# Performance work log

Hardware: AMD Instinct MI355X
Metric: run time of the kernel (lower is better)

## Reference

```python
import math
import jax, jax.numpy as jnp
import numpy as np

N = 100_000          # nodes
D = 128              # sample.num_node_features
E = 1_600_000        # edges (avg degree 16)
ACM = 4              # augmented_channels_multiplier
C = 128              # channels = 4*4*channels_optuna(=8)
RATIO = 0.7          # topk_ratio + 0.1
FINAL_NODES = 3


def setup_inputs() -> dict:
    key = jax.random.key(0)
    ks = jax.random.split(key, 14)
    s = 0.05
    x = jax.random.normal(ks[0], (N, D), jnp.float32)
    edge_index = jax.random.randint(ks[1], (2, E), 0, N, dtype=jnp.int32)
    # dense_input GraphConv(D, ACM): called with empty edges -> only lin_root weight + lin_rel bias matter
    Wd_root = jax.random.normal(ks[2], (ACM, D), jnp.float32) * s
    bd = jax.random.normal(ks[3], (ACM,), jnp.float32) * s
    # input GraphConv(ACM, C)
    Wi_rel = jax.random.normal(ks[4], (C, ACM), jnp.float32) * s
    bi = jax.random.normal(ks[5], (C,), jnp.float32) * s
    Wi_root = jax.random.normal(ks[6], (C, ACM), jnp.float32) * s
    # TopKPooling(C) attention vector
    p = jax.random.normal(ks[7], (C,), jnp.float32) * s
    # conv1 GraphConv(C, 2C)
    W1_rel = jax.random.normal(ks[8], (2 * C, C), jnp.float32) * s
    b1 = jax.random.normal(ks[9], (2 * C,), jnp.float32) * s
    W1_root = jax.random.normal(ks[10], (2 * C, C), jnp.float32) * s
    # output Linear(3 * 2C, 1)
    Wo = jax.random.normal(ks[11], (1, FINAL_NODES * 2 * C), jnp.float32) * s
    bo = jax.random.normal(ks[12], (1,), jnp.float32) * s
    return {"x": x, "edge_index": edge_index, "Wd_root": Wd_root, "bd": bd,
            "Wi_rel": Wi_rel, "bi": bi, "Wi_root": Wi_root, "p": p,
            "W1_rel": W1_rel, "b1": b1, "W1_root": W1_root, "Wo": Wo, "bo": bo}


def reference(x, edge_index, Wd_root, bd, Wi_rel, bi, Wi_root, p, W1_rel, b1, W1_root, Wo, bo):
    n = x.shape[0]
    src, dst = edge_index[0], edge_index[1]  # messages flow src -> dst

    # dense_input GraphConv with empty edge set: aggr == 0 -> lin_rel bias + lin_root(x)
    h = jax.nn.gelu(x @ Wd_root.T + bd, approximate=False)               # [N, ACM]

    # input GraphConv(ACM, C): out = lin_rel(sum_j x_j) + lin_root(x)
    aggr = jax.ops.segment_sum(h[src], dst, num_segments=n)              # [N, ACM]
    h = jax.nn.gelu(aggr @ Wi_rel.T + bi + h @ Wi_root.T, approximate=False)  # [N, C]

    # TopKPooling(C, ratio=0.7): score = tanh(x.p / ||p||), keep top-k, scale kept x by score
    k = int(math.ceil(RATIO * n))
    score = jnp.tanh((h @ p) / jnp.linalg.norm(p))                        # [N]
    top_scores, perm = jax.lax.top_k(score, k)
    hp = h[perm] * top_scores[:, None]                                    # [k, C]
    # remap edges: kept node -> new index, dropped -> sentinel k
    inv = jnp.full((n,), k, dtype=jnp.int32).at[perm].set(jnp.arange(k, dtype=jnp.int32))
    ns, nd = inv[src], inv[dst]
    valid = (ns < k) & (nd < k)

    # conv1 GraphConv(C, 2C) on coarsened graph (masked scatter, sentinel row dropped)
    msg = jnp.where(valid[:, None], hp[jnp.minimum(ns, k - 1)], 0.0)      # [E, C]
    aggr = jax.ops.segment_sum(msg, jnp.where(valid, nd, k), num_segments=k + 1)[:k]
    h2 = jax.nn.gelu(aggr @ W1_rel.T + b1 + hp @ W1_root.T, approximate=False)  # [k, 2C]

    # avg_pool_x with cluster = i % 3 over single-graph batch
    cluster = jnp.arange(k, dtype=jnp.int32) % FINAL_NODES
    sums = jax.ops.segment_sum(h2, cluster, num_segments=FINAL_NODES)
    counts = jax.ops.segment_sum(jnp.ones((k,), h2.dtype), cluster, num_segments=FINAL_NODES)
    pooled = sums / counts[:, None]                                       # [3, 2C]

    # output Linear on flattened vector -> shape [1]
    return pooled.reshape(-1) @ Wo.T + bo
```

## Files before the change

### kernel.cpp

```cpp
#include <hip/hip_runtime.h>
#include <stdint.h>

#define N_NODES 100000
#define D_FEAT  128
#define E_EDGES 1600000
#define ACMC    4
#define CCH     128
#define C2CH    256
#define KKEEP   70000
#define KPAD    70016
#define NBLK    547
#define BINCAP  64
#define NBINS   (1 << 20)
#define NWIN    8
#define WWIN    12500

#define NB_BUILD (1563 * NWIN)
#define NB_H1    (N_NODES / 4)
#define NB_WCONV 128
#define NB_FRONT (NB_BUILD + NB_H1 + NB_WCONV)

#define NB_GATHER ((N_NODES + 3) / 4)
#define NB_PACK   ((KPAD + 3) / 4)
#define NB_GP     (NB_GATHER + NB_PACK)

typedef unsigned int u32;
typedef unsigned long long u64;
typedef unsigned short u16;
typedef short bf16x8 __attribute__((ext_vector_type(8)));
typedef float f32x4 __attribute__((ext_vector_type(4)));
typedef int i32x4 __attribute__((ext_vector_type(4)));

__device__ __forceinline__ float gelu_exact(float v){
    return 0.5f * v * (1.0f + erff(v * 0.70710678118654752440f));
}
__device__ __forceinline__ float bflo(u32 v){ return __uint_as_float(v << 16); }
__device__ __forceinline__ float bfhi(u32 v){ return __uint_as_float(v & 0xFFFF0000u); }
__device__ __forceinline__ u16 f2bf(float f){
    u32 x = __float_as_uint(f);
    return (u16)((x + 0x7FFFu + ((x >> 16) & 1u)) >> 16);
}

__global__ __launch_bounds__(256) void k_front(const int* __restrict__ ei,
                                               int* __restrict__ deg,
                                               int* __restrict__ slot,
                                               const float* __restrict__ x,
                                               const float* __restrict__ Wd,
                                               const float* __restrict__ bd,
                                               float* __restrict__ h1,
                                               const float* __restrict__ Wrel,
                                               const float* __restrict__ Wroot,
                                               u16* __restrict__ wcat) {
    int b = blockIdx.x;
    if (b < NB_BUILD) {
        int win = b & (NWIN - 1);
        int chunk = b >> 3;
        int e0 = (chunk * 256 + threadIdx.x) * 4;
        if (e0 >= E_EDGES) return;
        i32x4 dv = __builtin_nontemporal_load((const i32x4*)(ei + E_EDGES + e0));
        i32x4 sv = __builtin_nontemporal_load((const i32x4*)(ei + e0));
        int lo = win * WWIN, hi = lo + WWIN;
        #pragma unroll
        for (int j = 0; j < 4; j++) {
            int d = dv[j];
            if (d >= lo && d < hi) {
                int pos = atomicAdd(&deg[d], 1);
                if (pos < BINCAP) slot[d * BINCAP + pos] = sv[j];
            }
        }
        return;
    }
    if (b < NB_BUILD + NB_H1) {
        int tid = threadIdx.x;
        int wid = tid >> 6, lane = tid & 63;
        int node = (b - NB_BUILD) * 4 + wid;
        const float2* xr = (const float2*)(x + (size_t)node * D_FEAT);
        float2 v = xr[lane];
        const float2* wd = (const float2*)Wd;
        float s[4];
        #pragma unroll
        for (int j = 0; j < 4; j++) {
            float2 w = wd[j * 64 + lane];
            s[j] = v.x * w.x + v.y * w.y;
        }
        #pragma unroll
        for (int off = 32; off > 0; off >>= 1) {
            #pragma unroll
            for (int j = 0; j < 4; j++) s[j] += __shfl_xor(s[j], off);
        }
        if (lane == 0) {
            float4 o;
            o.x = gelu_exact(s[0] + bd[0]);
            o.y = gelu_exact(s[1] + bd[1]);
            o.z = gelu_exact(s[2] + bd[2]);
            o.w = gelu_exact(s[3] + bd[3]);
            ((float4*)h1)[node] = o;
        }
        return;
    }
    {
        int g = (b - NB_BUILD - NB_H1) * 256 + threadIdx.x;
        int ch = g >> 7, t = g & 127;
        wcat[(size_t)ch * 256 + t]       = f2bf(Wrel[(size_t)ch * 128 + t]);
        wcat[(size_t)ch * 256 + 128 + t] = f2bf(Wroot[(size_t)ch * 128 + t]);
    }
}

__global__ __launch_bounds__(256) void k_aggr1g(const int* __restrict__ deg,
                                                const int* __restrict__ slot,
                                                const float* __restrict__ h1,
                                                float* __restrict__ aggr1) {
    int d = blockIdx.x * blockDim.x + threadIdx.x;
    if (d >= N_NODES) return;
    int cnt = deg[d]; if (cnt > BINCAP) cnt = BINCAP;
    int base = d * BINCAP;
    float4 acc = make_float4(0.f, 0.f, 0.f, 0.f);
    for (int i0 = 0; i0 < cnt; i0 += 8) {
        int m = cnt - i0; if (m > 8) m = 8;
        int ss[8];
        #pragma unroll
        for (int j = 0; j < 8; j++) {
            int sj = slot[base + i0 + j];
            ss[j] = (j < m) ? sj : 0;
        }
        float4 vv[8];
        #pragma unroll
        for (int j = 0; j < 8; j++) vv[j] = ((const float4*)h1)[ss[j]];
        #pragma unroll
        for (int j = 0; j < 8; j++) {
            float msk = (j < m) ? 1.f : 0.f;
            acc.x += msk * vv[j].x;
            acc.y += msk * vv[j].y;
            acc.z += msk * vv[j].z;
            acc.w += msk * vv[j].w;
        }
    }
    ((float4*)aggr1)[d] = acc;
}

__global__ __launch_bounds__(256) void k_h_score(const float* __restrict__ aggr1,
                                                 const float* __restrict__ h1,
                                                 const float* __restrict__ Wi_rel,
                                                 const float* __restrict__ bi,
                                                 const float* __restrict__ Wi_root,
                                                 const float* __restrict__ p,
                                                 u16* __restrict__ hsb,
                                                 u32* __restrict__ dkey,
                                                 int* __restrict__ hist) {
    __shared__ float4 swr[128], swo[128];
    __shared__ float sbi[128], spv[128];
    __shared__ float spred[2];
    __shared__ float red[2][2];
    __shared__ float sscore[2];
    int tid = threadIdx.x;
    if (tid < 128) {
        swr[tid] = ((const float4*)Wi_rel)[tid];
        swo[tid] = ((const float4*)Wi_root)[tid];
        sbi[tid] = bi[tid];
        spv[tid] = p[tid];
    }
    __syncthreads();
    if (tid < 128) {
        float pp = spv[tid] * spv[tid];
        #pragma unroll
        for (int off = 32; off > 0; off >>= 1) pp += __shfl_xor(pp, off);
        if ((tid & 63) == 0) spred[tid >> 6] = pp;
    }
    __syncthreads();
    float pnorm = sqrtf(spred[0] + spred[1]);

    int half = tid >> 7;
    int c = tid & 127;
    int wih = (tid >> 6) & 1;
    int lane = tid & 63;
    float4 wr = swr[c], wo = swo[c];
    float bic = sbi[c], pc = spv[c];

    for (int node = blockIdx.x * 2 + half; node < N_NODES; node += gridDim.x * 2) {
        float4 ag = ((const float4*)aggr1)[node];
        float4 hv = ((const float4*)h1)[node];
        float val = ag.x * wr.x + ag.y * wr.y + ag.z * wr.z + ag.w * wr.w
                  + hv.x * wo.x + hv.y * wo.y + hv.z * wo.z + hv.w * wo.w
                  + bic;
        float g = gelu_exact(val);
        float hp = g * pc;
        #pragma unroll
        for (int off = 32; off > 0; off >>= 1) hp += __shfl_xor(hp, off);
        if (lane == 0) red[half][wih] = hp;
        __syncthreads();
        if (c == 0) {
            float H = red[half][0] + red[half][1];
            float sc = tanhf(H / pnorm);
            sscore[half] = sc;
            u32 u = __float_as_uint(sc);
            u32 asc = (u & 0x80000000u) ? ~u : (u | 0x80000000u);
            u32 d = ~asc;
            dkey[node] = d;
            atomicAdd(&hist[d >> 12], 1);
        }
        __syncthreads();
        hsb[(size_t)node * CCH + c] = f2bf(g * sscore[half]);
        __syncthreads();
    }
}

__global__ __launch_bounds__(256) void k_escan1(const int* __restrict__ in,
                                                int* __restrict__ out,
                                                int* __restrict__ bsum,
                                                int n) {
    __shared__ int wsum[4];
    int tid = threadIdx.x;
    int lane = tid & 63, wave = tid >> 6;
    int base = blockIdx.x * 4096 + tid * 16;
    int o[16];
    #pragma unroll
    for (int i = 0; i < 16; i++) {
        int g = base + i;
        o[i] = (g < n) ? in[g] : 0;
    }
    int ex[16];
    int run = 0;
    #pragma unroll
    for (int i = 0; i < 16; i++) { ex[i] = run; run += o[i]; }
    int inc = run;
    #pragma unroll
    for (int off = 1; off < 64; off <<= 1) {
        int t = __shfl_up(inc, off);
        if (lane >= off) inc += t;
    }
    int wexc = inc - run;
    if (lane == 63) wsum[wave] = inc;
    __syncthreads();
    int wbase = 0;
    #pragma unroll
    for (int w = 0; w < 4; w++) wbase += (w < wave) ? wsum[w] : 0;
    int tbase = wbase + wexc;
    #pragma unroll
    for (int i = 0; i < 16; i++) {
        int g = base + i;
        if (g < n) out[g] = tbase + ex[i];
    }
    if (tid == 255) bsum[blockIdx.x] = wbase + inc;
}

__global__ __launch_bounds__(256) void k_escan2(int* __restrict__ bsum, int n) {
    __shared__ int wsum[4];
    int tid = threadIdx.x;
    int lane = tid & 63, wave = tid >> 6;
    int val = (tid < n) ? bsum[tid] : 0;
    int inc = val;
    #pragma unroll
    for (int off = 1; off < 64; off <<= 1) {
        int t = __shfl_up(inc, off);
        if (lane >= off) inc += t;
    }
    int wexc = inc - val;
    if (lane == 63) wsum[wave] = inc;
    __syncthreads();
    int wbase = 0;
    #pragma unroll
    for (int w = 0; w < 4; w++) wbase += (w < wave) ? wsum[w] : 0;
    if (tid < n) bsum[tid] = wbase + wexc;
}

__global__ __launch_bounds__(256) void k_escan3(int* __restrict__ out,
                                                const int* __restrict__ bsum,
                                                int n) {
    int add = bsum[blockIdx.x];
    int base = blockIdx.x * 4096 + threadIdx.x * 16;
    #pragma unroll
    for (int i = 0; i < 16; i++) {
        int g = base + i;
        if (g < n) out[g] += add;
    }
}

__global__ __launch_bounds__(256) void k_scatter(const u32* __restrict__ dkey,
                                                 int* __restrict__ cursor,
                                                 u64* __restrict__ out64) {
    int i = blockIdx.x * blockDim.x + threadIdx.x;
    if (i >= N_NODES) return;
    u32 d = dkey[i];
    int pos = atomicAdd(&cursor[d >> 12], 1);
    out64[pos] = (((u64)d) << 32) | (u32)i;
}

__global__ __launch_bounds__(256) void k_refine(const u64* __restrict__ out64,
                                                const int* __restrict__ cursor,
                                                const int* __restrict__ hist,
                                                int* __restrict__ rank,
                                                int* __restrict__ noder) {
    int pp = blockIdx.x * blockDim.x + threadIdx.x;
    if (pp >= N_NODES) return;
    u64 kp = out64[pp];
    u32 b = (u32)(kp >> 44);
    int end = cursor[b];
    int cnt = hist[b];
    int start = end - cnt;
    int r = start;
    if (cnt > 1) {
        int c = 0;
        for (int q = start; q < end; q++) c += (out64[q] < kp) ? 1 : 0;
        r = start + c;
    }
    int node = (int)(u32)kp;
    rank[node] = r;
    noder[r] = node;
}

__global__ __launch_bounds__(256) void k_gatherpack(const int* __restrict__ deg,
                                                    const int* __restrict__ slot,
                                                    const int* __restrict__ rank,
                                                    const int* __restrict__ noder,
                                                    const u32* __restrict__ hsb32,
                                                    u32* __restrict__ inb32) {
    int b = blockIdx.x;
    int tid = threadIdx.x;
    int wid = tid >> 6, lane = tid & 63;
    if (b < NB_GATHER) {
        int d = b * 4 + wid;
        if (d >= N_NODES) return;
        int rd = rank[d];
        if (rd >= KKEEP) return;
        int cnt = deg[d]; if (cnt > BINCAP) cnt = BINCAP;
        int base = d * BINCAP;
        float ax = 0.f, ay = 0.f;
        for (int i0 = 0; i0 < cnt; i0 += 16) {
            int m = cnt - i0; if (m > 16) m = 16;
            int ss[16];
            #pragma unroll
            for (int j = 0; j < 16; j++) {
                int sj = slot[base + i0 + j];
                ss[j] = (j < m) ? sj : 0;
            }
            int rr[16];
            u32 vv[16];
            #pragma unroll
            for (int j = 0; j < 16; j++) {
                rr[j] = rank[ss[j]];
                vv[j] = hsb32[(size_t)ss[j] * 64 + lane];
            }
            #pragma unroll
            for (int j = 0; j < 16; j++) {
                float msk = (j < m && rr[j] < KKEEP) ? 1.f : 0.f;
                ax += msk * bflo(vv[j]);
                ay += msk * bfhi(vv[j]);
            }
        }
        inb32[(size_t)rd * 128 + lane] = (u32)f2bf(ax) | ((u32)f2bf(ay) << 16);
        return;
    }
    {
        int r = (b - NB_GATHER) * 4 + wid;
        if (r >= KPAD) return;
        if (r < KKEEP) {
            int n = noder[r];
            inb32[(size_t)r * 128 + 64 + lane] = hsb32[(size_t)n * 64 + lane];
        } else {
            inb32[(size_t)r * 128 + lane] = 0;
            inb32[(size_t)r * 128 + 64 + lane] = 0;
        }
    }
}

__global__ __launch_bounds__(256, 2) void k_h2mfma(const u16* __restrict__ inb,
                                                   const u16* __restrict__ wcat,
                                                   const float* __restrict__ b1,
                                                   float* __restrict__ partial) {
    __shared__ u16 bs[128 * 256];
    __shared__ float ps[384];
    int tid = threadIdx.x;
    int rowt = blockIdx.x >> 1;
    int half = blockIdx.x & 1;
    int chbase = half * 128;

    {
        int lch = tid >> 1;
        int seg = tid & 1;
        const char* src = (const char*)wcat + (size_t)(chbase + lch) * 512 + seg * 256;
        char* dst = (char*)bs + (size_t)lch * 512;
        int swz = (lch & 7) << 4;
        #pragma unroll
        for (int i = 0; i < 16; i++) {
            int k = seg * 256 + i * 16;
            *(i32x4*)(dst + (k ^ swz)) = *(const i32x4*)(src + i * 16);
        }
    }
    for (int i = tid; i < 384; i += 256) ps[i] = 0.f;
    __syncthreads();

    int lane = tid & 63, wave = tid >> 6;
    int col = lane & 15, quad = lane >> 4;
    int rbase = rowt * 128 + wave * 32;

    bf16x8 a[2][8];
    #pragma unroll
    for (int m = 0; m < 2; m++) {
        const char* ar = (const char*)inb + (size_t)(rbase + m * 16 + col) * 512 + quad * 16;
        #pragma unroll
        for (int k0 = 0; k0 < 8; k0++)
            a[m][k0] = *(const bf16x8*)(ar + k0 * 64);
    }

    f32x4 acc[2][8];
    #pragma unroll
    for (int m = 0; m < 2; m++)
        #pragma unroll
        for (int n = 0; n < 8; n++)
            acc[m][n] = (f32x4){0.f, 0.f, 0.f, 0.f};

    int swzr = (col & 7) << 4;
    #pragma unroll
    for (int k0 = 0; k0 < 8; k0++) {
        int kb = k0 * 64 + quad * 16;
        bf16x8 b[8];
        #pragma unroll
        for (int n = 0; n < 8; n++) {
            int lch = n * 16 + col;
            b[n] = *(const bf16x8*)((const char*)bs + (size_t)lch * 512 + (kb ^ swzr));
        }
        #pragma unroll
        for (int n = 0; n < 8; n++) {
            acc[0][n] = __builtin_amdgcn_mfma_f32_16x16x32_bf16(a[0][k0], b[n], acc[0][n], 0, 0, 0);
            acc[1][n] = __builtin_amdgcn_mfma_f32_16x16x32_bf16(a[1][k0], b[n], acc[1][n], 0, 0, 0);
        }
    }

    #pragma unroll
    for (int m = 0; m < 2; m++) {
        #pragma unroll
        for (int n = 0; n < 8; n++) {
            int lch = n * 16 + col;
            float bias = b1[chbase + lch];
            float p0 = 0.f, p1 = 0.f, p2 = 0.f;
            #pragma unroll
            for (int reg = 0; reg < 4; reg++) {
                int r = rbase + m * 16 + quad * 4 + reg;
                float g = (r < KKEEP) ? gelu_exact(acc[m][n][reg] + bias) : 0.f;
                int md = r % 3;
                if (md == 0) p0 += g; else if (md == 1) p1 += g; else p2 += g;
            }
            p0 += __shfl_xor(p0, 16); p0 += __shfl_xor(p0, 32);
            p1 += __shfl_xor(p1, 16); p1 += __shfl_xor(p1, 32);
            p2 += __shfl_xor(p2, 16); p2 += __shfl_xor(p2, 32);
            if (quad == 0) {
                atomicAdd(&ps[0 * 128 + lch], p0);
                atomicAdd(&ps[1 * 128 + lch], p1);
                atomicAdd(&ps[2 * 128 + lch], p2);
            }
        }
    }
    __syncthreads();
    for (int i = tid; i < 384; i += 256)
        partial[(size_t)rowt * 768 + (i >> 7) * 256 + chbase + (i & 127)] = ps[i];
}

__global__ __launch_bounds__(256) void k_poolred(const float* __restrict__ partial,
                                                 float* __restrict__ pooled) {
    __shared__ float red[4][64];
    int tid = threadIdx.x, lane = tid & 63, wave = tid >> 6;
    int j = blockIdx.x * 64 + lane;
    float s = 0.f;
    for (int i = wave; i < NBLK; i += 4)
        s += partial[(size_t)i * 768 + j];
    red[wave][lane] = s;
    __syncthreads();
    if (wave == 0)
        pooled[j] = (red[0][lane] + red[1][lane]) + (red[2][lane] + red[3][lane]);
}

__global__ __launch_bounds__(768) void k_out(const float* __restrict__ pooled,
                                             const float* __restrict__ Wo,
                                             const float* __restrict__ bo,
                                             float* __restrict__ out) {
    __shared__ float red[12];
    int t = threadIdx.x;
    int ci = t >> 8;
    float cnt = (ci == 0) ? 23334.0f : 23333.0f;
    float acc = (pooled[t] / cnt) * Wo[t];
    #pragma unroll
    for (int off = 32; off > 0; off >>= 1) acc += __shfl_xor(acc, off);
    int wid = t >> 6, lane = t & 63;
    if (lane == 0) red[wid] = acc;
    __syncthreads();
    if (t == 0) {
        float s = 0.0f;
        #pragma unroll
        for (int w = 0; w < 12; w++) s += red[w];
        out[0] = s + bo[0];
    }
}

extern "C" void kernel_launch(void* const* d_in, const int* in_sizes, int n_in,
                              void* d_out, int out_size, void* d_ws, size_t ws_size,
                              hipStream_t stream) {
    const float* x       = (const float*)d_in[0];
    const int*   ei      = (const int*)d_in[1];
    const float* Wd      = (const float*)d_in[2];
    const float* bd      = (const float*)d_in[3];
    const float* Wi_rel  = (const float*)d_in[4];
    const float* bi      = (const float*)d_in[5];
    const float* Wi_root = (const float*)d_in[6];
    const float* p       = (const float*)d_in[7];
    const float* W1_rel  = (const float*)d_in[8];
    const float* b1      = (const float*)d_in[9];
    const float* W1_root = (const float*)d_in[10];
    const float* Wo      = (const float*)d_in[11];
    const float* bo      = (const float*)d_in[12];

    char* ws = (char*)d_ws;
    size_t off_b = 0;
    auto alloc = [&](size_t bytes) -> void* {
        void* ptr = ws + off_b;
        off_b += (bytes + 255) & ~(size_t)255;
        return ptr;
    };
    float* h1     = (float*)alloc((size_t)N_NODES * 4 * sizeof(float));
    float* aggr1  = (float*)alloc((size_t)N_NODES * 4 * sizeof(float));
    u16*   hsb    = (u16*)alloc((size_t)N_NODES * CCH * sizeof(u16));
    u32*   dkey   = (u32*)alloc((size_t)N_NODES * sizeof(u32));
    int*   rank   = (int*)alloc((size_t)N_NODES * sizeof(int));
    int*   noder  = (int*)alloc((size_t)N_NODES * sizeof(int));
    int*   deg    = (int*)alloc((size_t)N_NODES * sizeof(int));
    int*   slot   = (int*)alloc((size_t)N_NODES * BINCAP * sizeof(int));
    u16*   inb    = (u16*)alloc((size_t)KPAD * C2CH * sizeof(u16));
    u16*   wcat   = (u16*)alloc((size_t)C2CH * 256 * sizeof(u16));
    float* partial= (float*)alloc((size_t)NBLK * 768 * sizeof(float));
    float* pooled = (float*)alloc(768 * sizeof(float));
    (void)ws_size; (void)in_sizes; (void)n_in; (void)out_size;

    int* hist   = (int*)inb;
    int* cursor = (int*)inb + NBINS;
    u64* out64  = (u64*)((int*)inb + 2 * NBINS);
    int* bsum   = (int*)(out64 + N_NODES);

    hipMemsetAsync(deg, 0, (size_t)N_NODES * sizeof(int), stream);
    hipMemsetAsync(hist, 0, (size_t)NBINS * sizeof(int), stream);

    k_front<<<NB_FRONT, 256, 0, stream>>>(ei, deg, slot, x, Wd, bd, h1,
                                          W1_rel, W1_root, wcat);

    k_aggr1g<<<(N_NODES + 255) / 256, 256, 0, stream>>>(deg, slot, h1, aggr1);
    k_h_score<<<2048, 256, 0, stream>>>(aggr1, h1, Wi_rel, bi, Wi_root, p,
                                        hsb, dkey, hist);

    k_escan1<<<NBINS / 4096, 256, 0, stream>>>(hist, cursor, bsum, NBINS);
    k_escan2<<<1, 256, 0, stream>>>(bsum, 256);
    k_escan3<<<NBINS / 4096, 256, 0, stream>>>(cursor, bsum, NBINS);
    k_scatter<<<(N_NODES + 255) / 256, 256, 0, stream>>>(dkey, cursor, out64);
    k_refine<<<(N_NODES + 255) / 256, 256, 0, stream>>>(out64, cursor, hist, rank, noder);

    k_gatherpack<<<NB_GP, 256, 0, stream>>>(deg, slot, rank, noder,
                                            (const u32*)hsb, (u32*)inb);
    k_h2mfma<<<NBLK * 2, 256, 0, stream>>>(inb, wcat, b1, partial);
    k_poolred<<<12, 256, 0, stream>>>(partial, pooled);
    k_out<<<1, 768, 0, stream>>>(pooled, Wo, bo, (float*)d_out);
}
```

Before: 441.7 us.

## Zero dropped nodes' features in refine and interleave front-kernel block roles

k_refine now zeroes the bf16 feature rows of nodes ranked beyond the keep count. This lets k_gatherpack drop the per-edge rank lookup and mask only on slot count, removing one dependent random gather per edge. Separately, k_front interleaves edge-binning blocks with node-projection and weight-conversion blocks (every third block does binning) so atomic-heavy and bandwidth-heavy work share the GPU at the same time. The cost is extra 256-byte writes for about 30k dropped rows and hard-coded block-count constants.

Result: faster. 413.1 us (-6.5%).

```diff
diff --git a/kernel.cpp b/kernel.cpp
--- a/kernel.cpp
+++ b/kernel.cpp
@@ -15,10 +15,9 @@
 #define NWIN    8
 #define WWIN    12500
 
-#define NB_BUILD (1563 * NWIN)
-#define NB_H1    (N_NODES / 4)
-#define NB_WCONV 128
-#define NB_FRONT (NB_BUILD + NB_H1 + NB_WCONV)
+#define NB_BUILD 12504
+#define NB_OTHER 25128
+#define NB_FRONT 37632
 
 #define NB_GATHER ((N_NODES + 3) / 4)
 #define NB_PACK   ((KPAD + 3) / 4)
@@ -52,28 +51,35 @@
                                                const float* __restrict__ Wroot,
                                                u16* __restrict__ wcat) {
     int b = blockIdx.x;
-    if (b < NB_BUILD) {
-        int win = b & (NWIN - 1);
-        int chunk = b >> 3;
-        int e0 = (chunk * 256 + threadIdx.x) * 4;
-        if (e0 >= E_EDGES) return;
-        i32x4 dv = __builtin_nontemporal_load((const i32x4*)(ei + E_EDGES + e0));
-        i32x4 sv = __builtin_nontemporal_load((const i32x4*)(ei + e0));
-        int lo = win * WWIN, hi = lo + WWIN;
-        #pragma unroll
-        for (int j = 0; j < 4; j++) {
-            int d = dv[j];
-            if (d >= lo && d < hi) {
-                int pos = atomicAdd(&deg[d], 1);
-                if (pos < BINCAP) slot[d * BINCAP + pos] = sv[j];
+    int q = b / 3, r = b - q * 3;
+    int oidx;
+    if (r == 2) {
+        if (q < NB_BUILD) {
+            int win = q & (NWIN - 1);
+            int chunk = q >> 3;
+            int e0 = (chunk * 256 + threadIdx.x) * 4;
+            if (e0 >= E_EDGES) return;
+            i32x4 dv = __builtin_nontemporal_load((const i32x4*)(ei + E_EDGES + e0));
+            i32x4 sv = __builtin_nontemporal_load((const i32x4*)(ei + e0));
+            int lo = win * WWIN, hi = lo + WWIN;
+            #pragma unroll
+            for (int j = 0; j < 4; j++) {
+                int d = dv[j];
+                if (d >= lo && d < hi) {
+                    int pos = atomicAdd(&deg[d], 1);
+                    if (pos < BINCAP) slot[d * BINCAP + pos] = sv[j];
+                }
             }
-        }
-        return;
-    }
-    if (b < NB_BUILD + NB_H1) {
+            return;
+        }
+        oidx = 25088 + (q - NB_BUILD);
+    } else {
+        oidx = 2 * q + r;
+    }
+    if (oidx < 25000) {
         int tid = threadIdx.x;
         int wid = tid >> 6, lane = tid & 63;
-        int node = (b - NB_BUILD) * 4 + wid;
+        int node = oidx * 4 + wid;
         const float2* xr = (const float2*)(x + (size_t)node * D_FEAT);
         float2 v = xr[lane];
         const float2* wd = (const float2*)Wd;
@@ -99,7 +105,7 @@
         return;
     }
     {
-        int g = (b - NB_BUILD - NB_H1) * 256 + threadIdx.x;
+        int g = (oidx - 25000) * 256 + threadIdx.x;
         int ch = g >> 7, t = g & 127;
         wcat[(size_t)ch * 256 + t]       = f2bf(Wrel[(size_t)ch * 128 + t]);
         wcat[(size_t)ch * 256 + 128 + t] = f2bf(Wroot[(size_t)ch * 128 + t]);
@@ -289,7 +295,8 @@
                                                 const int* __restrict__ cursor,
                                                 const int* __restrict__ hist,
                                                 int* __restrict__ rank,
-                                                int* __restrict__ noder) {
+                                                int* __restrict__ noder,
+                                                u32* __restrict__ hsb32) {
     int pp = blockIdx.x * blockDim.x + threadIdx.x;
     if (pp >= N_NODES) return;
     u64 kp = out64[pp];
@@ -306,6 +313,12 @@
     int node = (int)(u32)kp;
     rank[node] = r;
     noder[r] = node;
+    if (r >= KKEEP) {
+        i32x4 z = {0, 0, 0, 0};
+        i32x4* rp = (i32x4*)(hsb32 + (size_t)node * 64);
+        #pragma unroll
+        for (int i = 0; i < 16; i++) rp[i] = z;
+    }
 }
 
 __global__ __launch_bounds__(256) void k_gatherpack(const int* __restrict__ deg,
@@ -333,16 +346,13 @@
                 int sj = slot[base + i0 + j];
                 ss[j] = (j < m) ? sj : 0;
             }
-            int rr[16];
             u32 vv[16];
             #pragma unroll
-            for (int j = 0; j < 16; j++) {
-                rr[j] = rank[ss[j]];
+            for (int j = 0; j < 16; j++)
                 vv[j] = hsb32[(size_t)ss[j] * 64 + lane];
-            }
             #pragma unroll
             for (int j = 0; j < 16; j++) {
-                float msk = (j < m && rr[j] < KKEEP) ? 1.f : 0.f;
+                float msk = (j < m) ? 1.f : 0.f;
                 ax += msk * bflo(vv[j]);
                 ay += msk * bfhi(vv[j]);
             }
@@ -548,7 +558,8 @@
     k_escan2<<<1, 256, 0, stream>>>(bsum, 256);
     k_escan3<<<NBINS / 4096, 256, 0, stream>>>(cursor, bsum, NBINS);
     k_scatter<<<(N_NODES + 255) / 256, 256, 0, stream>>>(dkey, cursor, out64);
-    k_refine<<<(N_NODES + 255) / 256, 256, 0, stream>>>(out64, cursor, hist, rank, noder);
+    k_refine<<<(N_NODES + 255) / 256, 256, 0, stream>>>(out64, cursor, hist,
+                                                        rank, noder, (u32*)hsb);
 
     k_gatherpack<<<NB_GP, 256, 0, stream>>>(deg, slot, rank, noder,
                                             (const u32*)hsb, (u32*)inb);
```
